# Optimization experiments

Measured on AMD Instinct MI355X. Metric: run time of the kernel, lower is better.

The kernel has to match this reference:

```python
import jax, jax.numpy as jnp
import numpy as np
import math

ORIG_FREQ = 16000
NEW_FREQ = 14400
LPW = 6           # lowpass_filter_width


def _filter_params():
    """Replicates Resample._indices_and_weights with numpy (static constants)."""
    base = math.gcd(ORIG_FREQ, NEW_FREQ)
    conv_stride = ORIG_FREQ // base          # input samples per unit
    output_samples = NEW_FREQ // base        # polyphase count P
    min_freq = min(ORIG_FREQ, NEW_FREQ)
    lc = 0.99 * 0.5 * min_freq               # lowpass cutoff
    ww = LPW / (2.0 * lc)                    # window half-width (seconds)
    output_t = np.arange(output_samples, dtype=np.float64) / NEW_FREQ
    min_i = np.ceil((output_t - ww) * ORIG_FREQ)
    max_i = np.floor((output_t + ww) * ORIG_FREQ)
    W = int((max_i - min_i + 1).max())       # max filter width
    j = np.arange(W, dtype=np.float64)
    input_index = min_i[:, None] + j[None, :]
    delta_t = input_index / ORIG_FREQ - output_t[:, None]
    weights = np.zeros_like(delta_t)
    inside = np.abs(delta_t) < ww
    weights[inside] = 0.5 * (1 + np.cos(2 * math.pi * lc / LPW * delta_t[inside]))
    zero = delta_t == 0.0
    nz = ~zero
    weights[nz] *= np.sin(2 * math.pi * lc * delta_t[nz]) / (math.pi * delta_t[nz])
    weights[zero] *= 2 * lc
    weights /= ORIG_FREQ
    return min_i.astype(np.int64), weights.astype(np.float32), output_samples, conv_stride


def _output_samples(n):
    """Replicates Resample._output_samples (LinearResample::GetNumOutputSamples)."""
    tick = ORIG_FREQ * NEW_FREQ // math.gcd(ORIG_FREQ, NEW_FREQ)
    interval = n * (tick // ORIG_FREQ)
    tpo = tick // NEW_FREQ
    last = interval // tpo
    if last * tpo == interval:
        last -= 1
    return last + 1


def setup_inputs() -> dict:
    key = jax.random.key(0)
    _, w, _, _ = _filter_params()
    waveforms = jax.random.normal(key, (16, 480000), dtype=jnp.float32)
    return {"waveforms": waveforms, "weights": jnp.asarray(w)}


def _resample(waveforms, weights):
    fi, _, P, stride = _filter_params()
    B, N = waveforms.shape
    W = weights.shape[1]
    tot = _output_samples(N)
    M = (tot - 1) // P + 1                   # conv outputs per phase
    left_pad = max(0, -int(fi.min()))
    need = int(fi.max()) + stride * (M - 1) + W
    right_pad = max(0, need - N)
    wav = jnp.pad(waveforms, ((0, 0), (left_pad, right_pad)))
    # output sample n = i + P*m (phase i, unit m) reads input window starting
    # at first_indices[i] + stride*m  -> static gather index table [P, M, W]
    idx = (fi[:, None, None] + left_pad
           + stride * np.arange(M, dtype=np.int64)[None, :, None]
           + np.arange(W, dtype=np.int64)[None, None, :]).astype(np.int32)
    g = wav[:, idx]                          # [B, P, M, W]
    out = jnp.einsum('bpmw,pw->bpm', g, weights)
    out = jnp.transpose(out, (0, 2, 1)).reshape(B, M * P)  # interleave phases
    return out[:, :tot]


def reference(waveforms, weights):
    return _resample(waveforms, weights)
```

## Files before the change

### kernel.cpp

```cpp
#include <hip/hip_runtime.h>


#define RS_TPB 256

__global__ __launch_bounds__(RS_TPB) void resample_kernel(
    const float* __restrict__ wav, const float* __restrict__ wgt,
    float* __restrict__ out, int N, int M, int TOT) {
  __shared__ __align__(16) float s_out[4][576];

  const int b = blockIdx.y;
  const int tid = threadIdx.x;
  const int w = tid >> 6;
  const int lane = tid & 63;
  const int wbase = blockIdx.x * RS_TPB + (w << 6);
  if (wbase >= M) return;

  const int m = wbase + lane;
  const float* __restrict__ wrow = wav + (size_t)b * N;

  const int gbase = 10 * m - 6;
  float win[24];
  if (gbase >= 0 && gbase + 24 <= N) {
#pragma unroll
    for (int r = 0; r < 12; ++r) {
      const float2 v = *reinterpret_cast<const float2*>(wrow + gbase + 2 * r);
      win[2 * r] = v.x;
      win[2 * r + 1] = v.y;
    }
  } else {
#pragma unroll
    for (int i = 0; i < 24; ++i) {
      const int gi = gbase + i;
      win[i] = (gi >= 0 && gi < N) ? wrow[gi] : 0.0f;
    }
  }

  const int OFF[9] = {0, 1, 2, 3, 4, 5, 6, 8, 9};
#pragma unroll
  for (int j = 0; j < 9; ++j) {
    const float* wp = &wgt[14 * j];
    float acc = 0.0f;
#pragma unroll
    for (int t = 0; t < 14; ++t) acc = fmaf(win[OFF[j] + t], wp[t], acc);
    s_out[w][lane * 9 + j] = acc;
  }
  __builtin_amdgcn_wave_barrier();

  float* __restrict__ orow = out + (size_t)b * TOT + (size_t)wbase * 9;
  const float4* so4 = reinterpret_cast<const float4*>(&s_out[w][0]);
#pragma unroll
  for (int it = 0; it < 3; ++it) {
    const int i4 = it * 64 + lane;
    if (i4 < 144) *reinterpret_cast<float4*>(orow + (i4 << 2)) = so4[i4];
  }
}

extern "C" void kernel_launch(void* const* d_in, const int* in_sizes, int n_in,
                              void* d_out, int out_size, void* d_ws, size_t ws_size,
                              hipStream_t stream) {
  const float* wav = (const float*)d_in[0];
  const float* wgt = (const float*)d_in[1];
  float* out = (float*)d_out;

  const int N = 480000;
  const int B = in_sizes[0] / N;
  const int TOT = out_size / B;
  const int M = (TOT + 8) / 9;

  dim3 grid((M + RS_TPB - 1) / RS_TPB, B);
  resample_kernel<<<grid, RS_TPB, 0, stream>>>(wav, wgt, out, N, M, TOT);
}
```

Measured before the change: 15.82 us.

## Stage input windows through LDS with async global_load_lds, two spans per wave

Each wave now handles two consecutive 64-unit spans and stages their input samples into LDS with asynchronous global-to-LDS loads, double-buffered so the second span's load overlaps the first span's compute. The grid is flattened to a 1D count of waves over batches. This replaces overlapping, unaligned per-lane float2 global loads with coalesced 16-byte loads. Edge spans fall back to a bounds-checked direct path. The hardcoded WPR constant and raw vmcnt waits tie the kernel to this exact input size and to the compiler's instruction ordering.

```diff
diff --git a/kernel.cpp b/kernel.cpp
--- a/kernel.cpp
+++ b/kernel.cpp
@@ -2,56 +2,112 @@
 
 
 #define RS_TPB 256
+#define WPR 375
+#define SPAN_F 768
+
+typedef __attribute__((address_space(1))) const void gvoid_t;
+typedef __attribute__((address_space(3))) void lvoid_t;
+
+__device__ __forceinline__ void fma_store(const float* win, float* sout,
+                                          const float* __restrict__ wgt,
+                                          float* __restrict__ orow, int lane) {
+  const int OFF[9] = {0, 1, 2, 3, 4, 5, 6, 8, 9};
+#pragma unroll
+  for (int j = 0; j < 9; ++j) {
+    float acc = 0.0f;
+#pragma unroll
+    for (int t = 0; t < 14; ++t)
+      acc = fmaf(win[OFF[j] + t], wgt[14 * j + t], acc);
+    sout[lane * 9 + j] = acc;
+  }
+  __builtin_amdgcn_wave_barrier();
+#pragma unroll
+  for (int it = 0; it < 3; ++it) {
+    const int i4 = it * 64 + lane;
+    if (i4 < 144) {
+      const float4 v = *reinterpret_cast<const float4*>(&sout[i4 << 2]);
+      *reinterpret_cast<float4*>(orow + (i4 << 2)) = v;
+    }
+  }
+  __builtin_amdgcn_wave_barrier();
+}
+
+__device__ __forceinline__ void compute_span_lds(const float* sin_buf,
+                                                 float* sout,
+                                                 const float* __restrict__ wgt,
+                                                 float* __restrict__ orow,
+                                                 int lane) {
+  float win[24];
+  const float2* s2 = reinterpret_cast<const float2*>(sin_buf);
+  const int d0 = 5 * lane + 5;
+#pragma unroll
+  for (int r = 0; r < 12; ++r) {
+    const float2 v = s2[d0 + r];
+    win[2 * r] = v.x;
+    win[2 * r + 1] = v.y;
+  }
+  fma_store(win, sout, wgt, orow, lane);
+}
+
+__device__ __forceinline__ void compute_span_direct(
+    int s, int lane, const float* __restrict__ wrow, int N, float* sout,
+    const float* __restrict__ wgt, float* __restrict__ orow) {
+  const int gbase = 640 * s + 10 * lane - 6;
+  float win[24];
+#pragma unroll
+  for (int i = 0; i < 24; ++i) {
+    const int gi = gbase + i;
+    win[i] = (gi >= 0 && gi < N) ? wrow[gi] : 0.0f;
+  }
+  fma_store(win, sout, wgt, orow, lane);
+}
 
 __global__ __launch_bounds__(RS_TPB) void resample_kernel(
     const float* __restrict__ wav, const float* __restrict__ wgt,
-    float* __restrict__ out, int N, int M, int TOT) {
+    float* __restrict__ out, int N, int TOT) {
+  __shared__ __align__(16) float s_in[4][2][SPAN_F];
   __shared__ __align__(16) float s_out[4][576];
 
-  const int b = blockIdx.y;
   const int tid = threadIdx.x;
   const int w = tid >> 6;
   const int lane = tid & 63;
-  const int wbase = blockIdx.x * RS_TPB + (w << 6);
-  if (wbase >= M) return;
+  const int gw = blockIdx.x * 4 + w;
+  const unsigned bu = (unsigned)gw / WPR;
+  const int pr = gw - (int)bu * WPR;
+  const int s0 = 2 * pr;
 
-  const int m = wbase + lane;
-  const float* __restrict__ wrow = wav + (size_t)b * N;
+  const float* __restrict__ wrow = wav + (size_t)bu * N;
+  float* __restrict__ obase = out + (size_t)bu * (size_t)TOT;
+  float* sout = &s_out[w][0];
 
-  const int gbase = 10 * m - 6;
-  float win[24];
-  if (gbase >= 0 && gbase + 24 <= N) {
+  if (pr > 0 && pr < WPR - 1) {
+    const int a0 = 640 * s0 - 16;
+    const int a1 = a0 + 640;
+    float* b0 = &s_in[w][0][0];
+    float* b1 = &s_in[w][1][0];
 #pragma unroll
-    for (int r = 0; r < 12; ++r) {
-      const float2 v = *reinterpret_cast<const float2*>(wrow + gbase + 2 * r);
-      win[2 * r] = v.x;
-      win[2 * r + 1] = v.y;
-    }
+    for (int it = 0; it < 3; ++it)
+      __builtin_amdgcn_global_load_lds(
+          (gvoid_t*)(wrow + a0 + it * 256 + lane * 4),
+          (lvoid_t*)(b0 + it * 256), 16, 0, 0);
+    __builtin_amdgcn_sched_barrier(0);
+#pragma unroll
+    for (int it = 0; it < 3; ++it)
+      __builtin_amdgcn_global_load_lds(
+          (gvoid_t*)(wrow + a1 + it * 256 + lane * 4),
+          (lvoid_t*)(b1 + it * 256), 16, 0, 0);
+    __builtin_amdgcn_sched_barrier(0);
+    asm volatile("s_waitcnt vmcnt(3)" ::: "memory");
+    __builtin_amdgcn_sched_barrier(0);
+    compute_span_lds(b0, sout, wgt, obase + (size_t)s0 * 576, lane);
+    asm volatile("s_waitcnt vmcnt(3)" ::: "memory");
+    __builtin_amdgcn_sched_barrier(0);
+    compute_span_lds(b1, sout, wgt, obase + (size_t)(s0 + 1) * 576, lane);
   } else {
-#pragma unroll
-    for (int i = 0; i < 24; ++i) {
-      const int gi = gbase + i;
-      win[i] = (gi >= 0 && gi < N) ? wrow[gi] : 0.0f;
-    }
-  }
-
-  const int OFF[9] = {0, 1, 2, 3, 4, 5, 6, 8, 9};
-#pragma unroll
-  for (int j = 0; j < 9; ++j) {
-    const float* wp = &wgt[14 * j];
-    float acc = 0.0f;
-#pragma unroll
-    for (int t = 0; t < 14; ++t) acc = fmaf(win[OFF[j] + t], wp[t], acc);
-    s_out[w][lane * 9 + j] = acc;
-  }
-  __builtin_amdgcn_wave_barrier();
-
-  float* __restrict__ orow = out + (size_t)b * TOT + (size_t)wbase * 9;
-  const float4* so4 = reinterpret_cast<const float4*>(&s_out[w][0]);
-#pragma unroll
-  for (int it = 0; it < 3; ++it) {
-    const int i4 = it * 64 + lane;
-    if (i4 < 144) *reinterpret_cast<float4*>(orow + (i4 << 2)) = so4[i4];
+    compute_span_direct(s0, lane, wrow, N, sout, wgt,
+                        obase + (size_t)s0 * 576);
+    compute_span_direct(s0 + 1, lane, wrow, N, sout, wgt,
+                        obase + (size_t)(s0 + 1) * 576);
   }
 }
 
@@ -65,8 +121,8 @@
   const int N = 480000;
   const int B = in_sizes[0] / N;
   const int TOT = out_size / B;
-  const int M = (TOT + 8) / 9;
+  const int n_waves = B * WPR;
+  dim3 grid(n_waves / 4);
 
-  dim3 grid((M + RS_TPB - 1) / RS_TPB, B);
-  resample_kernel<<<grid, RS_TPB, 0, stream>>>(wav, wgt, out, N, M, TOT);
+  resample_kernel<<<grid, RS_TPB, 0, stream>>>(wav, wgt, out, N, TOT);
 }
```

Result: slower. 17.66 us (+11.6%).
